# Optimization experiments

Hardware: AMD Instinct MI355X
Metric: run time of the kernel (lower is better)

Reference implementation:

```python
import jax, jax.numpy as jnp
import numpy as np

N = 160000          # active voxels / points
C = 128             # embed_channels
K = 27              # 3x3x3 submanifold conv kernel volume
NUM_CLUSTERS = 2048
BN_EPS = 1e-5


def setup_inputs() -> dict:
    key = jax.random.key(0)
    ks = jax.random.split(key, 16)
    s = 0.05
    inp = {
        "feat": jax.random.normal(ks[0], (N, C), jnp.float32),
        "cluster0": jax.random.randint(ks[1], (N,), 0, NUM_CLUSTERS, jnp.int32),
        "cluster1": jax.random.randint(ks[2], (N,), 0, NUM_CLUSTERS, jnp.int32),
        "cluster2": jax.random.randint(ks[3], (N,), 0, NUM_CLUSTERS, jnp.int32),
        "nbr_idx": jax.random.randint(ks[4], (N, K), 0, N, jnp.int32),
        "nbr_mask": jax.random.randint(ks[5], (N, K), 0, 2, jnp.int32) > 0,
        "lw_W": jax.random.normal(ks[6], (3, C, C), jnp.float32) * s,
        "lw_gamma": jnp.ones((3, C), jnp.float32),
        "lw_beta": jnp.zeros((3, C), jnp.float32),
        "w_W": jax.random.normal(ks[7], (3, C, C), jnp.float32) * s,
        "proj_W": jax.random.normal(ks[8], (4, C, C), jnp.float32) * s,
        "proj_gamma": jnp.ones((4, C), jnp.float32),
        "proj_beta": jnp.zeros((4, C), jnp.float32),
        "adaptive_W": jax.random.normal(ks[9], (C, 3), jnp.float32) * s,
        "fuse_W": jax.random.normal(ks[10], (2 * C, C), jnp.float32) * s,
        "fuse_gamma": jnp.ones((C,), jnp.float32),
        "fuse_beta": jnp.zeros((C,), jnp.float32),
        "conv_W": jax.random.normal(ks[11], (2, K, C, C), jnp.float32) * 0.02,
        "conv_gamma": jnp.ones((2, C), jnp.float32),
        "conv_beta": jnp.zeros((2, C), jnp.float32),
    }
    return inp


def _bn(x, gamma, beta):
    # BatchNorm1d, training mode: per-channel stats over points, biased var
    m = jnp.mean(x, axis=0)
    v = jnp.var(x, axis=0)
    return (x - m) * jax.lax.rsqrt(v + BN_EPS) * gamma + beta


def _seg_sum(x, seg):
    return jax.ops.segment_sum(x, seg, num_segments=NUM_CLUSTERS)


def _seg_mean(x, seg):
    s = _seg_sum(x, seg)
    cnt = jax.ops.segment_sum(jnp.ones((x.shape[0], 1), x.dtype), seg,
                              num_segments=NUM_CLUSTERS)
    return s / jnp.maximum(cnt, 1.0)


def _subm_conv(x, W, nbr_idx, nbr_mask):
    # submanifold 3x3x3 conv on active sites: masked gather + per-offset GEMM
    m = nbr_mask.astype(x.dtype)  # [N, K]
    out = jnp.zeros_like(x)
    for k in range(K):
        out = out + (x[nbr_idx[:, k]] * m[:, k:k + 1]) @ W[k]
    return out


def reference(feat, cluster0, cluster1, cluster2, nbr_idx, nbr_mask,
              lw_W, lw_gamma, lw_beta, w_W, proj_W, proj_gamma, proj_beta,
              adaptive_W, fuse_W, fuse_gamma, fuse_beta,
              conv_W, conv_gamma, conv_beta):
    clusters = [cluster0, cluster1, cluster2]
    feats = []
    for i, cl in enumerate(clusters):
        pw = jax.nn.relu(_bn(feat @ lw_W[i], lw_gamma[i], lw_beta[i]))
        pw = pw - _seg_mean(pw, cl)[cl]
        pw = pw @ w_W[i]
        pw = jnp.exp(pw - jnp.max(pw))                      # global max
        pw = pw / (_seg_sum(pw, cl)[cl] + 1e-6)
        pfeat = jax.nn.relu(_bn(feat @ proj_W[i], proj_gamma[i], proj_beta[i])) * pw
        pfeat = _seg_sum(pfeat, cl)[cl]
        feats.append(pfeat)

    adp = jax.nn.softmax(feat @ adaptive_W, axis=1)          # [N, 3]
    feats = jnp.stack(feats, axis=1)                         # [N, 3, C]
    fused_branch = jnp.einsum('ln,lnc->lc', adp, feats)

    f = jax.nn.relu(_bn(feat @ proj_W[3], proj_gamma[3], proj_beta[3]))
    f = jnp.concatenate([f, fused_branch], axis=1)           # [N, 2C]
    f = jax.nn.relu(_bn(f @ fuse_W, fuse_gamma, fuse_beta)) + feat

    res = f
    h = _subm_conv(f, conv_W[0], nbr_idx, nbr_mask)
    h = jax.nn.relu(_bn(h, conv_gamma[0], conv_beta[0]))
    h = _subm_conv(h, conv_W[1], nbr_idx, nbr_mask)
    h = _bn(h, conv_gamma[1], conv_beta[1])
    return jax.nn.relu(h + res)
```

## Files before the change

### kernel.cpp

```cpp
#include <hip/hip_runtime.h>
#include <stdint.h>

#define N_PTS 160000
#define C 128
#define K27 27
#define NCLU 2048
#define BN_EPS 1e-5f
#define KP 136
#define KP2 264

typedef float f32x4 __attribute__((ext_vector_type(4)));
typedef short s16x8 __attribute__((ext_vector_type(8)));

__device__ __forceinline__ float bf2f(unsigned short u){
  union { unsigned int i; float f; } v; v.i = ((unsigned int)u) << 16; return v.f;
}
__device__ __forceinline__ unsigned short f2bf(float f){
  union { float f; unsigned int i; } v; v.f = f;
  unsigned int u = v.i;
  u += 0x7FFFu + ((u >> 16) & 1u);
  return (unsigned short)(u >> 16);
}
__device__ __forceinline__ unsigned int pk(float a, float b){
  return (unsigned int)f2bf(a) | ((unsigned int)f2bf(b) << 16);
}
__device__ __forceinline__ void up2(int w, float& a, float& b){
  a = bf2f((unsigned short)(w & 0xFFFF));
  b = bf2f((unsigned short)(((unsigned int)w) >> 16));
}
__device__ __forceinline__ unsigned int encf(float f){
  union { float f; unsigned int i; } v; v.f = f;
  return ((int)v.i < 0) ? ~v.i : (v.i | 0x80000000u);
}
__device__ __forceinline__ float decf(unsigned int e){
  union { unsigned int i; float f; } v;
  v.i = ((int)e < 0) ? (e ^ 0x80000000u) : ~e;
  return v.f;
}
__device__ __forceinline__ void bn_coef(const float* st, const float* gamma, const float* beta,
                                        int c, float& sc, float& sh){
  float mean = st[c] * (1.0f / N_PTS);
  float var  = st[C + c] * (1.0f / N_PTS) - mean * mean;
  float g = gamma[c] * rsqrtf(fmaxf(var, 0.f) + BN_EPS);
  sc = g; sh = beta[c] - mean * g;
}

__global__ void k_prep_weights(const float* __restrict__ lw, const float* __restrict__ w,
                               const float* __restrict__ proj, const float* __restrict__ conv,
                               const float* __restrict__ fuse,
                               unsigned short* __restrict__ tlw, unsigned short* __restrict__ tw,
                               unsigned short* __restrict__ tproj, unsigned short* __restrict__ tconv,
                               unsigned short* __restrict__ tfuse)
{
  int z = blockIdx.x, tid = threadIdx.x;
  if (z < 64){
    const float* src; unsigned short* dst; bool swz = false;
    if (z < 3){ src = lw + z*16384; dst = tlw + z*16384; }
    else if (z < 6){ src = w + (z-3)*16384; dst = tw + (z-3)*16384; }
    else if (z < 10){ src = proj + (z-6)*16384; dst = tproj + (z-6)*16384; }
    else { src = conv + (z-10)*16384; dst = tconv + (z-10)*16384; swz = true; }
    for (int i = tid; i < 16384; i += 256){
      int n = i >> 7, k = i & 127;
      int pos = swz ? (n*128 + (((k >> 3) ^ (n & 7)) << 3) + (k & 7)) : i;
      dst[pos] = f2bf(src[k*128 + n]);
    }
  } else {
    for (int i = tid; i < 32768; i += 256){
      int n = i >> 8, k = i & 255;
      tfuse[i] = f2bf(fuse[k*128 + n]);
    }
  }
}

__global__ void k_detect_mask(const unsigned int* __restrict__ mw, int* __restrict__ mmode)
{
  __shared__ int flag;
  if (threadIdx.x == 0) flag = 0;
  __syncthreads();
  for (int i = threadIdx.x; i < 4096; i += 256)
    if (mw[i] > 1u) flag = 1;
  __syncthreads();
  if (threadIdx.x == 0) *mmode = flag;
}

__global__ void k_hist(const int* __restrict__ c0, const int* __restrict__ c1,
                       const int* __restrict__ c2, int* __restrict__ hist)
{
  int idx = blockIdx.x*blockDim.x + threadIdx.x;
  int stride = gridDim.x*blockDim.x;
  for (; idx < 3*N_PTS; idx += stride){
    int j = idx / N_PTS, r = idx - j*N_PTS;
    const int* cp = (j==0)?c0:((j==1)?c1:c2);
    atomicAdd(&hist[j*NCLU + cp[r]], 1);
  }
}

__global__ void k_prefix(const int* __restrict__ hist, int* __restrict__ starts,
                         int* __restrict__ cursor)
{
  int j = blockIdx.x, tid = threadIdx.x;
  __shared__ int buf[NCLU];
  __shared__ int csum[256];
  for (int i = tid; i < NCLU; i += 256) buf[i] = hist[j*NCLU + i];
  __syncthreads();
  int s = 0;
  #pragma unroll
  for (int k = 0; k < 8; k++) s += buf[tid*8 + k];
  csum[tid] = s;
  __syncthreads();
  if (tid == 0){
    int run = 0;
    for (int i = 0; i < 256; i++){ int t = csum[i]; csum[i] = run; run += t; }
  }
  __syncthreads();
  int acc = csum[tid];
  #pragma unroll
  for (int k = 0; k < 8; k++){
    int i = tid*8 + k;
    starts[j*(NCLU+1) + i] = acc;
    cursor[j*NCLU + i] = acc;
    acc += buf[i];
  }
  if (tid == 255) starts[j*(NCLU+1) + NCLU] = acc;
}

__global__ void k_scatter(const int* __restrict__ c0, const int* __restrict__ c1,
                          const int* __restrict__ c2, int* __restrict__ cursor,
                          int* __restrict__ perm)
{
  int idx = blockIdx.x*blockDim.x + threadIdx.x;
  int stride = gridDim.x*blockDim.x;
  for (; idx < 3*N_PTS; idx += stride){
    int j = idx / N_PTS, r = idx - j*N_PTS;
    const int* cp = (j==0)?c0:((j==1)?c1:c2);
    int cl = cp[r];
    int slot = atomicAdd(&cursor[j*NCLU + cl], 1);
    perm[j*N_PTS + slot] = r;
  }
}

template<int V>
__global__ void k_seg(const unsigned short* __restrict__ X,
                      const int* __restrict__ perm, const int* __restrict__ starts,
                      const float* __restrict__ st, const float* __restrict__ gamma,
                      const float* __restrict__ beta, float* __restrict__ S)
{
  __shared__ float red[16*128];
  const int cl = blockIdx.x;
  const int p0 = starts[cl], p1 = starts[cl+1];
  const int g = threadIdx.x >> 4, s = threadIdx.x & 15;
  const int c0 = s * 8;
  float sc[8], sh[8];
  #pragma unroll
  for (int j = 0; j < 8; j++) bn_coef(st, gamma, beta, c0 + j, sc[j], sh[j]);
  float acc[8];
  #pragma unroll
  for (int j = 0; j < 8; j++) acc[j] = 0.f;
  for (int p = p0 + g; p < p1; p += 16){
    int row = perm[p];
    int4 v = *(const int4*)(X + (size_t)row*C + c0);
    float f[8];
    up2(v.x, f[0], f[1]); up2(v.y, f[2], f[3]); up2(v.z, f[4], f[5]); up2(v.w, f[6], f[7]);
    #pragma unroll
    for (int j = 0; j < 8; j++) acc[j] += fmaxf(f[j]*sc[j] + sh[j], 0.f);
  }
  #pragma unroll
  for (int j = 0; j < 8; j++) red[g*128 + c0 + j] = acc[j];
  __syncthreads();
  if (threadIdx.x < 128){
    float t = 0.f;
    #pragma unroll
    for (int gg = 0; gg < 16; gg++) t += red[gg*128 + threadIdx.x];
    S[cl*C + threadIdx.x] = t;
  }
}

__global__ void k_seg12(const unsigned short* __restrict__ XP, const unsigned short* __restrict__ X2,
                        const int* __restrict__ perm, const int* __restrict__ starts,
                        const float* __restrict__ st, const float* __restrict__ gamma,
                        const float* __restrict__ beta, const unsigned int* __restrict__ genc,
                        float* __restrict__ S3)
{
  __shared__ float red[16*128];
  const int cl = blockIdx.x;
  const int p0 = starts[cl], p1 = starts[cl+1];
  const int g = threadIdx.x >> 4, s = threadIdx.x & 15;
  const int c0 = s * 8;
  const float gm = decf(*genc);
  float sc[8], sh[8];
  #pragma unroll
  for (int j = 0; j < 8; j++) bn_coef(st, gamma, beta, c0 + j, sc[j], sh[j]);

  float acc[8];
  #pragma unroll
  for (int j = 0; j < 8; j++) acc[j] = 0.f;
  for (int p = p0 + g; p < p1; p += 16){
    int row = perm[p];
    int4 v2 = *(const int4*)(X2 + (size_t)row*C + c0);
    float x2[8];
    up2(v2.x, x2[0], x2[1]); up2(v2.y, x2[2], x2[3]); up2(v2.z, x2[4], x2[5]); up2(v2.w, x2[6], x2[7]);
    #pragma unroll
    for (int j = 0; j < 8; j++) acc[j] += __expf(x2[j] - gm);
  }
  #pragma unroll
  for (int j = 0; j < 8; j++) red[g*128 + c0 + j] = acc[j];
  __syncthreads();
  if (threadIdx.x < 128){
    float t = 0.f;
    #pragma unroll
    for (int gg = 0; gg < 16; gg++) t += red[gg*128 + threadIdx.x];
    red[threadIdx.x] = t;
  }
  __syncthreads();
  float den[8];
  #pragma unroll
  for (int j = 0; j < 8; j++) den[j] = red[c0 + j] + 1e-6f;
  __syncthreads();

  #pragma unroll
  for (int j = 0; j < 8; j++) acc[j] = 0.f;
  for (int p = p0 + g; p < p1; p += 16){
    int row = perm[p];
    int4 v  = *(const int4*)(XP + (size_t)row*C + c0);
    int4 v2 = *(const int4*)(X2 + (size_t)row*C + c0);
    float f[8], x2[8];
    up2(v.x, f[0], f[1]); up2(v.y, f[2], f[3]); up2(v.z, f[4], f[5]); up2(v.w, f[6], f[7]);
    up2(v2.x, x2[0], x2[1]); up2(v2.y, x2[2], x2[3]); up2(v2.z, x2[4], x2[5]); up2(v2.w, x2[6], x2[7]);
    #pragma unroll
    for (int j = 0; j < 8; j++)
      acc[j] += fmaxf(f[j]*sc[j] + sh[j], 0.f) * __expf(x2[j] - gm) / den[j];
  }
  #pragma unroll
  for (int j = 0; j < 8; j++) red[g*128 + c0 + j] = acc[j];
  __syncthreads();
  if (threadIdx.x < 128){
    float t = 0.f;
    #pragma unroll
    for (int gg = 0; gg < 16; gg++) t += red[gg*128 + threadIdx.x];
    S3[cl*C + threadIdx.x] = t;
  }
}

__global__ void k_adp(const float* __restrict__ feat, const float* __restrict__ aW,
                      float* __restrict__ adp, unsigned short* __restrict__ featb)
{
  __shared__ float wsh[384];
  int tid = threadIdx.x;
  for (int i = tid; i < 384; i += 256) wsh[i] = aW[i];
  __syncthreads();
  int gidx = blockIdx.x*256 + tid;
  int stride = gridDim.x*256;
  for (int t4 = gidx; t4 < N_PTS*4; t4 += stride){
    int row = t4 >> 2, part = t4 & 3;
    float e0=0.f, e1=0.f, e2=0.f;
    const float* fr = feat + (size_t)row*C + part*32;
    unsigned int pb[16];
    #pragma unroll
    for (int c = 0; c < 32; c += 4){
      float4 v = *(const float4*)(fr + c);
      int cc = part*32 + c;
      e0 += v.x*wsh[cc*3+0] + v.y*wsh[(cc+1)*3+0] + v.z*wsh[(cc+2)*3+0] + v.w*wsh[(cc+3)*3+0];
      e1 += v.x*wsh[cc*3+1] + v.y*wsh[(cc+1)*3+1] + v.z*wsh[(cc+2)*3+1] + v.w*wsh[(cc+3)*3+1];
      e2 += v.x*wsh[cc*3+2] + v.y*wsh[(cc+1)*3+2] + v.z*wsh[(cc+2)*3+2] + v.w*wsh[(cc+3)*3+2];
      pb[(c>>1)]   = pk(v.x, v.y);
      pb[(c>>1)+1] = pk(v.z, v.w);
    }
    if (featb){
      int4* dst = (int4*)(featb + (size_t)row*C + part*32);
      dst[0] = make_int4(pb[0], pb[1], pb[2], pb[3]);
      dst[1] = make_int4(pb[4], pb[5], pb[6], pb[7]);
      dst[2] = make_int4(pb[8], pb[9], pb[10], pb[11]);
      dst[3] = make_int4(pb[12], pb[13], pb[14], pb[15]);
    }
    e0 += __shfl_xor(e0, 1); e0 += __shfl_xor(e0, 2);
    e1 += __shfl_xor(e1, 1); e1 += __shfl_xor(e1, 2);
    e2 += __shfl_xor(e2, 1); e2 += __shfl_xor(e2, 2);
    if (part == 0){
      float m = fmaxf(e0, fmaxf(e1, e2));
      float p0 = __expf(e0-m), p1 = __expf(e1-m), p2 = __expf(e2-m);
      float inv = 1.f/(p0+p1+p2);
      adp[row*3+0] = p0*inv; adp[row*3+1] = p1*inv; adp[row*3+2] = p2*inv;
    }
  }
}

__device__ __forceinline__ void gemm_stats_epi(float* csum, float* csq, float* sred,
                                               int wave, int l4, int l16, int tid,
                                               float* __restrict__ stats)
{
  #pragma unroll
  for (int t = 0; t < 8; t++){
    csum[t] += __shfl_xor(csum[t], 16); csum[t] += __shfl_xor(csum[t], 32);
    csq[t]  += __shfl_xor(csq[t], 16);  csq[t]  += __shfl_xor(csq[t], 32);
  }
  if (l4 == 0){
    #pragma unroll
    for (int t = 0; t < 8; t++){
      sred[wave*128 + t*16 + l16] = csum[t];
      sred[512 + wave*128 + t*16 + l16] = csq[t];
    }
  }
  __syncthreads();
  if (tid < 128){
    float s = 0.f, q = 0.f;
    #pragma unroll
    for (int w2 = 0; w2 < 4; w2++){ s += sred[w2*128 + tid]; q += sred[512 + w2*128 + tid]; }
    atomicAdd(&stats[tid], s);
    atomicAdd(&stats[C + tid], q);
  }
}

template<typename AT>
__device__ __forceinline__ void stage_A(const AT* __restrict__ A, unsigned short* As,
                                        int row0, int r, int s)
{
  #pragma unroll
  for (int p = 0; p < 4; p++){
    int rr = r + p * 16;
    if constexpr (sizeof(AT) == 2){
      *(int4*)(As + rr * KP + s * 8) =
        *(const int4*)((const unsigned short*)A + (size_t)(row0 + rr) * C + s * 8);
    } else {
      const float4* ap = (const float4*)((const float*)A + (size_t)(row0 + rr) * C + s * 8);
      float4 x = ap[0], y = ap[1];
      *(int4*)(As + rr * KP + s * 8) =
        make_int4(pk(x.x,x.y), pk(x.z,x.w), pk(y.x,y.y), pk(y.z,y.w));
    }
  }
}

template<typename AT>
__global__ __launch_bounds__(256, 3)
void k_gemm_plain(const AT* __restrict__ A, const unsigned short* __restrict__ Bt,
                  unsigned short* __restrict__ Out, float* __restrict__ stats)
{
  __shared__ unsigned short As[64 * KP];
  __shared__ unsigned short Bs[128 * KP];
  const int tid = threadIdx.x;
  const int row0 = blockIdx.x * 64;
  const int r = tid >> 4, s = tid & 15;
  stage_A<AT>(A, As, row0, r, s);
  #pragma unroll
  for (int p = 0; p < 8; p++){
    int nn = r + p * 16;
    *(int4*)(Bs + nn * KP + s * 8) = *(const int4*)(Bt + nn * C + s * 8);
  }
  __syncthreads();
  const int lane = tid & 63, wave = tid >> 6;
  const int l16 = lane & 15, l4 = lane >> 4, m0 = wave * 16;
  f32x4 acc[8];
  #pragma unroll
  for (int t = 0; t < 8; t++) acc[t] = (f32x4){0.f,0.f,0.f,0.f};
  #pragma unroll
  for (int kk = 0; kk < 4; kk++){
    s16x8 a = *(const s16x8*)(As + (m0 + l16) * KP + kk * 32 + l4 * 8);
    #pragma unroll
    for (int t = 0; t < 8; t++){
      s16x8 b = *(const s16x8*)(Bs + (t * 16 + l16) * KP + kk * 32 + l4 * 8);
      acc[t] = __builtin_amdgcn_mfma_f32_16x16x32_bf16(a, b, acc[t], 0, 0, 0);
    }
  }
  float csum[8], csq[8];
  #pragma unroll
  for (int t = 0; t < 8; t++){
    float ss = 0.f, qq = 0.f;
    #pragma unroll
    for (int q = 0; q < 4; q++){
      float v = acc[t][q];
      int grow = row0 + m0 + l4 * 4 + q;
      Out[(size_t)grow * C + t * 16 + l16] = f2bf(v);
      ss += v; qq += v*v;
    }
    csum[t] = ss; csq[t] = qq;
  }
  __syncthreads();
  gemm_stats_epi(csum, csq, (float*)As, wave, l4, l16, tid, stats);
}

template<typename AT>
__global__ __launch_bounds__(256, 3)
void k_gemm_dual(const AT* __restrict__ A,
                 const unsigned short* __restrict__ Bt0, const unsigned short* __restrict__ Bt1,
                 unsigned short* __restrict__ Out0, unsigned short* __restrict__ Out1,
                 float* __restrict__ stats0, float* __restrict__ stats1)
{
  __shared__ unsigned short As[64 * KP];
  __shared__ unsigned short Bs[128 * KP];
  const int tid = threadIdx.x;
  const int row0 = blockIdx.x * 64;
  const int r = tid >> 4, s = tid & 15;
  const int lane = tid & 63, wave = tid >> 6;
  const int l16 = lane & 15, l4 = lane >> 4, m0 = wave * 16;

  stage_A<AT>(A, As, row0, r, s);
  #pragma unroll
  for (int p = 0; p < 8; p++){
    int nn = r + p * 16;
    *(int4*)(Bs + nn * KP + s * 8) = *(const int4*)(Bt0 + nn * C + s * 8);
  }
  __syncthreads();

  f32x4 acc[8];
  float csum0[8], csq0[8], csum1[8], csq1[8];

  #pragma unroll
  for (int t = 0; t < 8; t++) acc[t] = (f32x4){0.f,0.f,0.f,0.f};
  #pragma unroll
  for (int kk = 0; kk < 4; kk++){
    s16x8 a = *(const s16x8*)(As + (m0 + l16) * KP + kk * 32 + l4 * 8);
    #pragma unroll
    for (int t = 0; t < 8; t++){
      s16x8 b = *(const s16x8*)(Bs + (t * 16 + l16) * KP + kk * 32 + l4 * 8);
      acc[t] = __builtin_amdgcn_mfma_f32_16x16x32_bf16(a, b, acc[t], 0, 0, 0);
    }
  }
  #pragma unroll
  for (int t = 0; t < 8; t++){
    float ss = 0.f, qq = 0.f;
    #pragma unroll
    for (int q = 0; q < 4; q++){
      float v = acc[t][q];
      int grow = row0 + m0 + l4 * 4 + q;
      Out0[(size_t)grow * C + t * 16 + l16] = f2bf(v);
      ss += v; qq += v*v;
    }
    csum0[t] = ss; csq0[t] = qq;
  }
  __syncthreads();
  #pragma unroll
  for (int p = 0; p < 8; p++){
    int nn = r + p * 16;
    *(int4*)(Bs + nn * KP + s * 8) = *(const int4*)(Bt1 + nn * C + s * 8);
  }
  __syncthreads();

  #pragma unroll
  for (int t = 0; t < 8; t++) acc[t] = (f32x4){0.f,0.f,0.f,0.f};
  #pragma unroll
  for (int kk = 0; kk < 4; kk++){
    s16x8 a = *(const s16x8*)(As + (m0 + l16) * KP + kk * 32 + l4 * 8);
    #pragma unroll
    for (int t = 0; t < 8; t++){
      s16x8 b = *(const s16x8*)(Bs + (t * 16 + l16) * KP + kk * 32 + l4 * 8);
      acc[t] = __builtin_amdgcn_mfma_f32_16x16x32_bf16(a, b, acc[t], 0, 0, 0);
    }
  }
  #pragma unroll
  for (int t = 0; t < 8; t++){
    float ss = 0.f, qq = 0.f;
    #pragma unroll
    for (int q = 0; q < 4; q++){
      float v = acc[t][q];
      int grow = row0 + m0 + l4 * 4 + q;
      Out1[(size_t)grow * C + t * 16 + l16] = f2bf(v);
      ss += v; qq += v*v;
    }
    csum1[t] = ss; csq1[t] = qq;
  }
  __syncthreads();
  gemm_stats_epi(csum0, csq0, (float*)As, wave, l4, l16, tid, stats0);
  __syncthreads();
  gemm_stats_epi(csum1, csq1, (float*)As, wave, l4, l16, tid, stats1);
}

__global__ __launch_bounds__(256, 3)
void k_gemm_center(const unsigned short* __restrict__ PW, const unsigned short* __restrict__ Bt,
                   const int* __restrict__ cla, const float* __restrict__ S1,
                   const int* __restrict__ cnt, const float* __restrict__ st,
                   const float* __restrict__ gamma, const float* __restrict__ beta,
                   unsigned short* __restrict__ Out, unsigned int* __restrict__ gmax)
{
  __shared__ unsigned short As[64 * KP];
  __shared__ unsigned short Bs[128 * KP];
  __shared__ float wred[4];
  const int tid = threadIdx.x;
  const int row0 = blockIdx.x * 64;
  const int r = tid >> 4, s = tid & 15;
  float sc[8], sh[8];
  #pragma unroll
  for (int j = 0; j < 8; j++) bn_coef(st, gamma, beta, s*8 + j, sc[j], sh[j]);
  #pragma unroll
  for (int p = 0; p < 4; p++){
    int rr = r + p * 16;
    int grow = row0 + rr;
    int cl = cla[grow];
    float inv = 1.f / fmaxf(1.f, (float)cnt[cl]);
    int4 v = *(const int4*)(PW + (size_t)grow * C + s * 8);
    const float4* mp = (const float4*)(S1 + cl * C + s * 8);
    float4 ma = mp[0], mb = mp[1];
    float f[8];
    up2(v.x, f[0], f[1]); up2(v.y, f[2], f[3]); up2(v.z, f[4], f[5]); up2(v.w, f[6], f[7]);
    float m8[8] = {ma.x,ma.y,ma.z,ma.w,mb.x,mb.y,mb.z,mb.w};
    float o[8];
    #pragma unroll
    for (int j = 0; j < 8; j++) o[j] = fmaxf(f[j]*sc[j] + sh[j], 0.f) - m8[j]*inv;
    *(int4*)(As + rr * KP + s * 8) = make_int4(pk(o[0],o[1]), pk(o[2],o[3]), pk(o[4],o[5]), pk(o[6],o[7]));
  }
  #pragma unroll
  for (int p = 0; p < 8; p++){
    int nn = r + p * 16;
    *(int4*)(Bs + nn * KP + s * 8) = *(const int4*)(Bt + nn * C + s * 8);
  }
  __syncthreads();
  const int lane = tid & 63, wave = tid >> 6;
  const int l16 = lane & 15, l4 = lane >> 4, m0 = wave * 16;
  f32x4 acc[8];
  #pragma unroll
  for (int t = 0; t < 8; t++) acc[t] = (f32x4){0.f,0.f,0.f,0.f};
  #pragma unroll
  for (int kk = 0; kk < 4; kk++){
    s16x8 a = *(const s16x8*)(As + (m0 + l16) * KP + kk * 32 + l4 * 8);
    #pragma unroll
    for (int t = 0; t < 8; t++){
      s16x8 b = *(const s16x8*)(Bs + (t * 16 + l16) * KP + kk * 32 + l4 * 8);
      acc[t] = __builtin_amdgcn_mfma_f32_16x16x32_bf16(a, b, acc[t], 0, 0, 0);
    }
  }
  float mx = -3.4e38f;
  #pragma unroll
  for (int t = 0; t < 8; t++){
    #pragma unroll
    for (int q = 0; q < 4; q++){
      int grow = row0 + m0 + l4 * 4 + q;
      unsigned short ob = f2bf(acc[t][q]);
      Out[(size_t)grow * C + t * 16 + l16] = ob;
      mx = fmaxf(mx, bf2f(ob));
    }
  }
  #pragma unroll
  for (int off = 32; off; off >>= 1) mx = fmaxf(mx, __shfl_xor(mx, off));
  if ((tid & 63) == 0) wred[tid >> 6] = mx;
  __syncthreads();
  if (tid == 0){
    float m = fmaxf(fmaxf(wred[0], wred[1]), fmaxf(wred[2], wred[3]));
    atomicMax(gmax, encf(m));
  }
}

__global__ __launch_bounds__(256, 2)
void k_gemm_fuse(const unsigned short* __restrict__ XP3, const float* __restrict__ adp,
                 const int* __restrict__ cl0, const int* __restrict__ cl1,
                 const int* __restrict__ cl2, const float* __restrict__ S3,
                 const float* __restrict__ st, const float* __restrict__ gamma,
                 const float* __restrict__ beta, const unsigned short* __restrict__ Bt,
                 unsigned short* __restrict__ Out, float* __restrict__ stats)
{
  __shared__ unsigned short As[64 * KP2];
  __shared__ unsigned short Bs[128 * KP];
  __shared__ float scs[C], shs[C];
  const int tid = threadIdx.x;
  if (tid < C){ float a, b; bn_coef(st, gamma, beta, tid, a, b); scs[tid] = a; shs[tid] = b; }
  __syncthreads();
  const int row0 = blockIdx.x * 64;
  const int r8 = tid >> 5, s = tid & 31;
  const int r = tid >> 4, s16i = tid & 15;
  #pragma unroll
  for (int p = 0; p < 8; p++){
    int rr = r8 + p * 8;
    int grow = row0 + rr;
    if (s < 16){
      int c0 = s * 8;
      int4 v = *(const int4*)(XP3 + (size_t)grow * C + c0);
      float f0,f1,f2,f3,f4,f5,f6,f7;
      up2(v.x,f0,f1); up2(v.y,f2,f3); up2(v.z,f4,f5); up2(v.w,f6,f7);
      float o0 = fmaxf(f0*scs[c0+0]+shs[c0+0],0.f), o1 = fmaxf(f1*scs[c0+1]+shs[c0+1],0.f);
      float o2 = fmaxf(f2*scs[c0+2]+shs[c0+2],0.f), o3 = fmaxf(f3*scs[c0+3]+shs[c0+3],0.f);
      float o4 = fmaxf(f4*scs[c0+4]+shs[c0+4],0.f), o5 = fmaxf(f5*scs[c0+5]+shs[c0+5],0.f);
      float o6 = fmaxf(f6*scs[c0+6]+shs[c0+6],0.f), o7 = fmaxf(f7*scs[c0+7]+shs[c0+7],0.f);
      *(int4*)(As + rr * KP2 + c0) = make_int4(pk(o0,o1), pk(o2,o3), pk(o4,o5), pk(o6,o7));
    } else {
      int c0 = (s - 16) * 8;
      float a0 = adp[grow*3+0], a1 = adp[grow*3+1], a2 = adp[grow*3+2];
      const float* p0 = S3 + (size_t)cl0[grow] * C + c0;
      const float* p1 = S3 + (size_t)NCLU * C + (size_t)cl1[grow] * C + c0;
      const float* p2 = S3 + (size_t)2 * NCLU * C + (size_t)cl2[grow] * C + c0;
      float o[8];
      #pragma unroll
      for (int j = 0; j < 8; j++) o[j] = a0*p0[j] + a1*p1[j] + a2*p2[j];
      *(int4*)(As + rr * KP2 + 128 + c0) = make_int4(pk(o[0],o[1]), pk(o[2],o[3]), pk(o[4],o[5]), pk(o[6],o[7]));
    }
  }
  const int lane = tid & 63, wave = tid >> 6;
  const int l16 = lane & 15, l4 = lane >> 4, m0 = wave * 16;
  f32x4 acc[8];
  #pragma unroll
  for (int t = 0; t < 8; t++) acc[t] = (f32x4){0.f,0.f,0.f,0.f};
  #pragma unroll
  for (int h = 0; h < 2; h++){
    if (h) __syncthreads();
    #pragma unroll
    for (int p = 0; p < 8; p++){
      int nn = r + p * 16;
      *(int4*)(Bs + nn * KP + s16i * 8) = *(const int4*)(Bt + nn * 256 + h * 128 + s16i * 8);
    }
    __syncthreads();
    #pragma unroll
    for (int kk = 0; kk < 4; kk++){
      s16x8 a = *(const s16x8*)(As + (m0 + l16) * KP2 + h * 128 + kk * 32 + l4 * 8);
      #pragma unroll
      for (int t = 0; t < 8; t++){
        s16x8 b = *(const s16x8*)(Bs + (t * 16 + l16) * KP + kk * 32 + l4 * 8);
        acc[t] = __builtin_amdgcn_mfma_f32_16x16x32_bf16(a, b, acc[t], 0, 0, 0);
      }
    }
  }
  float csum[8], csq[8];
  #pragma unroll
  for (int t = 0; t < 8; t++){
    float ss = 0.f, qq = 0.f;
    #pragma unroll
    for (int q = 0; q < 4; q++){
      float v = acc[t][q];
      int grow = row0 + m0 + l4 * 4 + q;
      Out[(size_t)grow * C + t * 16 + l16] = f2bf(v);
      ss += v; qq += v*v;
    }
    csum[t] = ss; csq[t] = qq;
  }
  __syncthreads();
  gemm_stats_epi(csum, csq, (float*)As, wave, l4, l16, tid, stats);
}

__device__ __forceinline__ int ld_midx(const int* __restrict__ nbr, const void* __restrict__ maskp,
                                       int mm, int g){
  bool on = mm ? (((const unsigned char*)maskp)[g] != 0)
               : (((const int*)maskp)[g] != 0);
  int v = nbr[g];
  return on ? v : -1;
}

template<typename OT>
__global__ __launch_bounds__(512, 4)
void k_conv(const unsigned short* __restrict__ In, const unsigned short* __restrict__ Wt,
            const int* __restrict__ nbr, const void* __restrict__ maskp,
            const int* __restrict__ mmode, OT* __restrict__ Out, float* __restrict__ stats)
{
  __shared__ unsigned short Bs[2][128*128];
  const int tid = threadIdx.x;
  const int lane = tid & 63, wave = tid >> 6;
  const int l16 = lane & 15, l4 = lane >> 4;
  const int row0 = blockIdx.x * 128;
  const int mm = *mmode;
  const int rg = row0 + wave*16 + l16;
  const s16x8 z8 = (s16x8){0,0,0,0,0,0,0,0};

  auto stage_B = [&](int buf, int k){
    const char* gsrc = (const char*)(Wt + k*16384);
    char* lbase = (char*)&Bs[buf][0];
    #pragma unroll
    for (int p = 0; p < 4; p++){
      int chunk = p*512 + wave*64;
      __builtin_amdgcn_global_load_lds(
        (const unsigned int*)(gsrc + (size_t)(chunk + lane)*16),
        (unsigned int*)(lbase + (size_t)chunk*16), 16, 0, 0);
    }
  };

  f32x4 acc[8];
  #pragma unroll
  for (int t = 0; t < 8; t++) acc[t] = (f32x4){0.f,0.f,0.f,0.f};

  s16x8 A0[4], A1[4];
  auto gather = [&](s16x8* dA, int gi){
    #pragma unroll
    for (int kk = 0; kk < 4; kk++)
      dA[kk] = (gi >= 0) ? *(const s16x8*)(In + (size_t)gi*C + kk*32 + l4*8) : z8;
  };
  auto compute = [&](const s16x8* a, int buf){
    #pragma unroll
    for (int kk = 0; kk < 4; kk++){
      #pragma unroll
      for (int t = 0; t < 8; t++){
        int n = t*16 + l16;
        s16x8 b = *(const s16x8*)(&Bs[buf][n*128 + ((((kk<<2)|l4) ^ (n & 7)) << 3)]);
        acc[t] = __builtin_amdgcn_mfma_f32_16x16x32_bf16(a[kk], b, acc[t], 0, 0, 0);
      }
    }
  };

  stage_B(0, 0);
  int i0 = ld_midx(nbr, maskp, mm, rg*K27 + 0);
  gather(A0, i0);
  i0 = ld_midx(nbr, maskp, mm, rg*K27 + 1);
  __syncthreads();

  #pragma unroll 1
  for (int kb = 0; kb < 13; kb++){
    const int k = kb * 2;
    stage_B(1, k + 1);
    gather(A1, i0);
    i0 = ld_midx(nbr, maskp, mm, rg*K27 + k + 2);
    compute(A0, 0);
    __syncthreads();
    stage_B(0, k + 2);
    gather(A0, i0);
    if (kb < 12) i0 = ld_midx(nbr, maskp, mm, rg*K27 + k + 3);
    compute(A1, 1);
    __syncthreads();
  }
  compute(A0, 0);

  float csum[8], csq[8];
  #pragma unroll
  for (int t = 0; t < 8; t++){
    float ss = 0.f, qq = 0.f;
    #pragma unroll
    for (int q = 0; q < 4; q++){
      float v = acc[t][q];
      int grow = row0 + wave*16 + l4*4 + q;
      if constexpr (sizeof(OT) == 2) Out[(size_t)grow * C + t*16 + l16] = f2bf(v);
      else                           Out[(size_t)grow * C + t*16 + l16] = v;
      ss += v; qq += v*v;
    }
    csum[t] = ss; csq[t] = qq;
  }
  #pragma unroll
  for (int t = 0; t < 8; t++){
    csum[t] += __shfl_xor(csum[t], 16); csum[t] += __shfl_xor(csum[t], 32);
    csq[t]  += __shfl_xor(csq[t], 16);  csq[t]  += __shfl_xor(csq[t], 32);
  }
  __syncthreads();
  float* sred = (float*)Bs;
  if (l4 == 0){
    #pragma unroll
    for (int t = 0; t < 8; t++){
      sred[wave*128 + t*16 + l16] = csum[t];
      sred[1024 + wave*128 + t*16 + l16] = csq[t];
    }
  }
  __syncthreads();
  if (tid < 128){
    float s = 0.f, q = 0.f;
    #pragma unroll
    for (int w2 = 0; w2 < 8; w2++){ s += sred[w2*128 + tid]; q += sred[1024 + w2*128 + tid]; }
    atomicAdd(&stats[tid], s);
    atomicAdd(&stats[C + tid], q);
  }
}

template<int RELU>
__global__ void k_bnapply(const unsigned short* __restrict__ X, unsigned short* __restrict__ Y,
                          const float* __restrict__ st, const float* __restrict__ gamma,
                          const float* __restrict__ beta)
{
  const int total = N_PTS * 16;
  for (int idx = blockIdx.x*blockDim.x + threadIdx.x; idx < total; idx += gridDim.x*blockDim.x){
    int c0 = (idx & 15) * 8;
    int4 v = *(const int4*)(X + (size_t)idx * 8);
    float f[8];
    up2(v.x, f[0], f[1]); up2(v.y, f[2], f[3]); up2(v.z, f[4], f[5]); up2(v.w, f[6], f[7]);
    float o[8];
    #pragma unroll
    for (int j = 0; j < 8; j++){
      float sc, sh; bn_coef(st, gamma, beta, c0 + j, sc, sh);
      float t = f[j] * sc + sh;
      if (RELU) t = fmaxf(t, 0.f);
      o[j] = t;
    }
    *(int4*)(Y + (size_t)idx * 8) = make_int4(pk(o[0],o[1]), pk(o[2],o[3]), pk(o[4],o[5]), pk(o[6],o[7]));
  }
}

__global__ void k_fres(const unsigned short* __restrict__ G, const float* __restrict__ st,
                       const float* __restrict__ gamma, const float* __restrict__ beta,
                       const float* __restrict__ feat, unsigned short* __restrict__ FB)
{
  const int total = N_PTS * 16;
  for (int idx = blockIdx.x*blockDim.x + threadIdx.x; idx < total; idx += gridDim.x*blockDim.x){
    int c0 = (idx & 15) * 8;
    int4 v = *(const int4*)(G + (size_t)idx * 8);
    float f[8];
    up2(v.x, f[0], f[1]); up2(v.y, f[2], f[3]); up2(v.z, f[4], f[5]); up2(v.w, f[6], f[7]);
    const float4* fp = (const float4*)(feat + (size_t)idx * 8);
    float4 fa = fp[0], fb4 = fp[1];
    float fe[8] = {fa.x,fa.y,fa.z,fa.w,fb4.x,fb4.y,fb4.z,fb4.w};
    float o[8];
    #pragma unroll
    for (int j = 0; j < 8; j++){
      float sc, sh; bn_coef(st, gamma, beta, c0 + j, sc, sh);
      o[j] = fmaxf(f[j]*sc + sh, 0.f) + fe[j];
    }
    *(int4*)(FB + (size_t)idx * 8) = make_int4(pk(o[0],o[1]), pk(o[2],o[3]), pk(o[4],o[5]), pk(o[6],o[7]));
  }
}

__global__ void k_final(float* __restrict__ H2, const float* __restrict__ st,
                        const float* __restrict__ gamma, const float* __restrict__ beta,
                        const unsigned short* __restrict__ FB)
{
  const int total = N_PTS * 16;
  for (int idx = blockIdx.x*blockDim.x + threadIdx.x; idx < total; idx += gridDim.x*blockDim.x){
    int c0 = (idx & 15) * 8;
    float4* hp = (float4*)(H2 + (size_t)idx * 8);
    float4 a = hp[0], b = hp[1];
    int4 vf = *(const int4*)(FB + (size_t)idx * 8);
    float fr[8];
    up2(vf.x, fr[0], fr[1]); up2(vf.y, fr[2], fr[3]); up2(vf.z, fr[4], fr[5]); up2(vf.w, fr[6], fr[7]);
    float h[8] = {a.x,a.y,a.z,a.w,b.x,b.y,b.z,b.w};
    #pragma unroll
    for (int j = 0; j < 8; j++){
      float sc, sh; bn_coef(st, gamma, beta, c0 + j, sc, sh);
      h[j] = fmaxf(h[j]*sc + sh + fr[j], 0.f);
    }
    hp[0] = make_float4(h[0],h[1],h[2],h[3]);
    hp[1] = make_float4(h[4],h[5],h[6],h[7]);
  }
}

extern "C" void kernel_launch(void* const* d_in, const int* in_sizes, int n_in,
                              void* d_out, int out_size, void* d_ws, size_t ws_size,
                              hipStream_t stream)
{
  (void)in_sizes; (void)n_in; (void)out_size;
  const float* feat   = (const float*)d_in[0];
  const int* cls[3]   = {(const int*)d_in[1], (const int*)d_in[2], (const int*)d_in[3]};
  const int* nbr      = (const int*)d_in[4];
  const void* mask    = d_in[5];
  const float* lw_W   = (const float*)d_in[6];
  const float* lw_g   = (const float*)d_in[7];
  const float* lw_b   = (const float*)d_in[8];
  const float* w_W    = (const float*)d_in[9];
  const float* proj_W = (const float*)d_in[10];
  const float* proj_g = (const float*)d_in[11];
  const float* proj_b = (const float*)d_in[12];
  const float* adW    = (const float*)d_in[13];
  const float* fuse_W = (const float*)d_in[14];
  const float* fuse_g = (const float*)d_in[15];
  const float* fuse_b = (const float*)d_in[16];
  const float* conv_W = (const float*)d_in[17];
  const float* conv_g = (const float*)d_in[18];
  const float* conv_b = (const float*)d_in[19];

  char* w = (char*)d_ws;
  float*          stats  = (float*)(w + 0);
  unsigned int*   gmax   = (unsigned int*)(w + 10240);
  int*            mmode  = (int*)(w + 10240 + 16);
  int*            hist   = (int*)(w + 10496);
  int*            starts = (int*)(w + 35072);
  int*            cursor = (int*)(w + 59904);
  int*            perm   = (int*)(w + 84480);
  float*          S1     = (float*)(w + 2004480);
  float*          S3     = (float*)(w + 4101632);
  float*          adp    = (float*)(w + 7247360);
  unsigned short* tlw    = (unsigned short*)(w + 9167360);
  unsigned short* tw     = (unsigned short*)(w + 9265664);
  unsigned short* tproj  = (unsigned short*)(w + 9363968);
  unsigned short* tfuse  = (unsigned short*)(w + 9495040);
  unsigned short* tconv  = (unsigned short*)(w + 9560576);
  unsigned short* B1     = (unsigned short*)(w + 11330048);
  unsigned short* B2     = (unsigned short*)(w + 52290048);
  unsigned short* B3     = (unsigned short*)(w + 93250048);
  const bool useb = ws_size >= (size_t)175170048;
  unsigned short* featb = useb ? (unsigned short*)(w + 134210048) : nullptr;

  hipMemsetAsync(d_ws, 0, 35072, stream);

  k_prep_weights<<<65, 256, 0, stream>>>(lw_W, w_W, proj_W, conv_W, fuse_W,
                                         tlw, tw, tproj, tconv, tfuse);
  k_detect_mask<<<1, 256, 0, stream>>>((const unsigned int*)mask, mmode);
  k_hist<<<1024, 256, 0, stream>>>(cls[0], cls[1], cls[2], hist);
  k_prefix<<<3, 256, 0, stream>>>(hist, starts, cursor);
  k_scatter<<<1024, 256, 0, stream>>>(cls[0], cls[1], cls[2], cursor, perm);
  k_adp<<<2500, 256, 0, stream>>>(feat, adW, adp, featb);

  if (useb) k_gemm_plain<unsigned short><<<2500, 256, 0, stream>>>(featb, tlw, B1, stats);
  else      k_gemm_plain<float><<<2500, 256, 0, stream>>>(feat, tlw, B1, stats);

  for (int i = 0; i < 3; i++){
    k_seg<0><<<2048, 256, 0, stream>>>(B1, perm + i*N_PTS, starts + i*(NCLU+1),
                                       stats + i*256, lw_g + i*C, lw_b + i*C, S1);
    k_gemm_center<<<2500, 256, 0, stream>>>(B1, tw + i*16384, cls[i], S1, hist + i*NCLU,
                                            stats + i*256, lw_g + i*C, lw_b + i*C, B3, gmax + i);
    const unsigned short* w0 = tproj + i*16384;
    const unsigned short* w1 = (i < 2) ? (tlw + (i+1)*16384) : (tproj + 3*16384);
    float* st1 = (i < 2) ? (stats + (i+1)*256) : (stats + 6*256);
    if (useb) k_gemm_dual<unsigned short><<<2500, 256, 0, stream>>>(featb, w0, w1, B2, B1,
                                                                    stats + (3+i)*256, st1);
    else      k_gemm_dual<float><<<2500, 256, 0, stream>>>(feat, w0, w1, B2, B1,
                                                           stats + (3+i)*256, st1);
    k_seg12<<<2048, 256, 0, stream>>>(B2, B3, perm + i*N_PTS, starts + i*(NCLU+1),
                                      stats + (3+i)*256, proj_g + i*C, proj_b + i*C,
                                      gmax + i, S3 + (size_t)i*NCLU*C);
  }

  k_gemm_fuse<<<2500, 256, 0, stream>>>(B1, adp, cls[0], cls[1], cls[2], S3,
                                        stats + 6*256, proj_g + 3*C, proj_b + 3*C, tfuse,
                                        B2, stats + 7*256);
  k_fres<<<2048, 256, 0, stream>>>(B2, stats + 7*256, fuse_g, fuse_b, feat, B3);

  k_conv<unsigned short><<<1250, 512, 0, stream>>>(B3, tconv, nbr, mask, mmode, B1, stats + 8*256);
  k_bnapply<1><<<2048, 256, 0, stream>>>(B1, B2, stats + 8*256, conv_g, conv_b);
  k_conv<float><<<1250, 512, 0, stream>>>(B2, tconv + 27*16384, nbr, mask, mmode,
                                          (float*)d_out, stats + 9*256);
  k_final<<<2048, 256, 0, stream>>>((float*)d_out, stats + 9*256, conv_g + C, conv_b + C, B3);
}
```

Before: 1.286 ms.

## Double rows per wave in submanifold conv to reuse LDS weight tiles

```diff
diff --git a/kernel.cpp b/kernel.cpp
--- a/kernel.cpp
+++ b/kernel.cpp
@@ -639,9 +639,10 @@
   const int tid = threadIdx.x;
   const int lane = tid & 63, wave = tid >> 6;
   const int l16 = lane & 15, l4 = lane >> 4;
-  const int row0 = blockIdx.x * 128;
+  const int row0 = blockIdx.x * 256;
   const int mm = *mmode;
-  const int rg = row0 + wave*16 + l16;
+  const int r0g = row0 + wave*32 + l16;
+  const int r1g = r0g + 16;
   const s16x8 z8 = (s16x8){0,0,0,0,0,0,0,0};
 
   auto stage_B = [&](int buf, int k){
@@ -656,49 +657,54 @@
     }
   };
 
-  f32x4 acc[8];
-  #pragma unroll
-  for (int t = 0; t < 8; t++) acc[t] = (f32x4){0.f,0.f,0.f,0.f};
+  f32x4 acc0[8], acc1[8];
+  #pragma unroll
+  for (int t = 0; t < 8; t++){ acc0[t] = (f32x4){0.f,0.f,0.f,0.f}; acc1[t] = (f32x4){0.f,0.f,0.f,0.f}; }
 
   s16x8 A0[4], A1[4];
-  auto gather = [&](s16x8* dA, int gi){
-    #pragma unroll
-    for (int kk = 0; kk < 4; kk++)
-      dA[kk] = (gi >= 0) ? *(const s16x8*)(In + (size_t)gi*C + kk*32 + l4*8) : z8;
+  auto gather = [&](int gi0, int gi1){
+    #pragma unroll
+    for (int kk = 0; kk < 4; kk++){
+      A0[kk] = (gi0 >= 0) ? *(const s16x8*)(In + (size_t)gi0*C + kk*32 + l4*8) : z8;
+      A1[kk] = (gi1 >= 0) ? *(const s16x8*)(In + (size_t)gi1*C + kk*32 + l4*8) : z8;
+    }
   };
-  auto compute = [&](const s16x8* a, int buf){
+  auto compute = [&](int buf){
     #pragma unroll
     for (int kk = 0; kk < 4; kk++){
       #pragma unroll
       for (int t = 0; t < 8; t++){
         int n = t*16 + l16;
         s16x8 b = *(const s16x8*)(&Bs[buf][n*128 + ((((kk<<2)|l4) ^ (n & 7)) << 3)]);
-        acc[t] = __builtin_amdgcn_mfma_f32_16x16x32_bf16(a[kk], b, acc[t], 0, 0, 0);
+        acc0[t] = __builtin_amdgcn_mfma_f32_16x16x32_bf16(A0[kk], b, acc0[t], 0, 0, 0);
+        acc1[t] = __builtin_amdgcn_mfma_f32_16x16x32_bf16(A1[kk], b, acc1[t], 0, 0, 0);
       }
     }
   };
 
   stage_B(0, 0);
-  int i0 = ld_midx(nbr, maskp, mm, rg*K27 + 0);
-  gather(A0, i0);
-  i0 = ld_midx(nbr, maskp, mm, rg*K27 + 1);
+  int i0 = ld_midx(nbr, maskp, mm, r0g*K27 + 0);
+  int i1 = ld_midx(nbr, maskp, mm, r1g*K27 + 0);
   __syncthreads();
 
   #pragma unroll 1
   for (int kb = 0; kb < 13; kb++){
     const int k = kb * 2;
     stage_B(1, k + 1);
-    gather(A1, i0);
-    i0 = ld_midx(nbr, maskp, mm, rg*K27 + k + 2);
-    compute(A0, 0);
+    gather(i0, i1);
+    i0 = ld_midx(nbr, maskp, mm, r0g*K27 + k + 1);
+    i1 = ld_midx(nbr, maskp, mm, r1g*K27 + k + 1);
+    compute(0);
     __syncthreads();
     stage_B(0, k + 2);
-    gather(A0, i0);
-    if (kb < 12) i0 = ld_midx(nbr, maskp, mm, rg*K27 + k + 3);
-    compute(A1, 1);
+    gather(i0, i1);
+    i0 = ld_midx(nbr, maskp, mm, r0g*K27 + k + 2);
+    i1 = ld_midx(nbr, maskp, mm, r1g*K27 + k + 2);
+    compute(1);
     __syncthreads();
   }
-  compute(A0, 0);
+  gather(i0, i1);
+  compute(0);
 
   float csum[8], csq[8];
   #pragma unroll
@@ -706,8 +712,16 @@
     float ss = 0.f, qq = 0.f;
     #pragma unroll
     for (int q = 0; q < 4; q++){
-      float v = acc[t][q];
-      int grow = row0 + wave*16 + l4*4 + q;
+      float v = acc0[t][q];
+      int grow = row0 + wave*32 + l4*4 + q;
+      if constexpr (sizeof(OT) == 2) Out[(size_t)grow * C + t*16 + l16] = f2bf(v);
+      else                           Out[(size_t)grow * C + t*16 + l16] = v;
+      ss += v; qq += v*v;
+    }
+    #pragma unroll
+    for (int q = 0; q < 4; q++){
+      float v = acc1[t][q];
+      int grow = row0 + wave*32 + 16 + l4*4 + q;
       if constexpr (sizeof(OT) == 2) Out[(size_t)grow * C + t*16 + l16] = f2bf(v);
       else                           Out[(size_t)grow * C + t*16 + l16] = v;
       ss += v; qq += v*v;
@@ -888,9 +902,9 @@
                                         B2, stats + 7*256);
   k_fres<<<2048, 256, 0, stream>>>(B2, stats + 7*256, fuse_g, fuse_b, feat, B3);
 
-  k_conv<unsigned short><<<1250, 512, 0, stream>>>(B3, tconv, nbr, mask, mmode, B1, stats + 8*256);
+  k_conv<unsigned short><<<625, 512, 0, stream>>>(B3, tconv, nbr, mask, mmode, B1, stats + 8*256);
   k_bnapply<1><<<2048, 256, 0, stream>>>(B1, B2, stats + 8*256, conv_g, conv_b);
-  k_conv<float><<<1250, 512, 0, stream>>>(B2, tconv + 27*16384, nbr, mask, mmode,
-                                          (float*)d_out, stats + 9*256);
+  k_conv<float><<<625, 512, 0, stream>>>(B2, tconv + 27*16384, nbr, mask, mmode,
+                                         (float*)d_out, stats + 9*256);
   k_final<<<2048, 256, 0, stream>>>((float*)d_out, stats + 9*256, conv_g + C, conv_b + C, B3);
 }
```

Result: slower. 1.597 ms (+24.2%).
